# Kernel optimization log

Measured on AMD Instinct MI355X. Metric: run time of the kernel, lower is better.

The kernel has to match this reference:

```python
import jax, jax.numpy as jnp
import numpy as np

K = 4          # deform conv kernel size
STRIDE = 4     # deform conv stride (no padding)
EPS = 1e-5     # BatchNorm eps
SLOPE = 0.01   # LeakyReLU default negative slope


def conv2d(x, w, b, stride):
    out = jax.lax.conv_general_dilated(
        x, w, (stride, stride), 'VALID',
        dimension_numbers=('NCHW', 'OIHW', 'NCHW'))
    return out + b[None, :, None, None]


def batchnorm(x, g, b, m, v):
    inv = g / jnp.sqrt(v + EPS)
    return x * inv[None, :, None, None] + (b - m * inv)[None, :, None, None]


def leaky_relu(x):
    return jnp.where(x >= 0, x, SLOPE * x)


def deform_conv(x, offset, w, b):
    # x: [B,C,H,W], offset: [B,2*K*K,Ho,Wo] with (dy,dx) interleaved per kernel tap
    B, C, H, W = x.shape
    Ho, Wo = offset.shape[2], offset.shape[3]
    KK = K * K
    off = offset.reshape(B, KK, 2, Ho, Wo)
    kh = jnp.repeat(jnp.arange(K), K).astype(x.dtype)   # [KK] kernel row
    kw = jnp.tile(jnp.arange(K), K).astype(x.dtype)     # [KK] kernel col
    base_y = (jnp.arange(Ho) * STRIDE).astype(x.dtype)
    base_x = (jnp.arange(Wo) * STRIDE).astype(x.dtype)
    # sampling coordinates [B,KK,Ho,Wo]
    py = base_y[None, None, :, None] + kh[None, :, None, None] + off[:, :, 0]
    px = base_x[None, None, None, :] + kw[None, :, None, None] + off[:, :, 1]
    y0 = jnp.floor(py)
    x0 = jnp.floor(px)
    wy = py - y0
    wx = px - x0

    def corner(yc, xc):
        yi = yc.astype(jnp.int32)
        xi = xc.astype(jnp.int32)
        valid = (yi >= 0) & (yi < H) & (xi >= 0) & (xi < W)
        yi = jnp.clip(yi, 0, H - 1)
        xi = jnp.clip(xi, 0, W - 1)
        # per-batch gather: [B,C,KK,Ho,Wo]
        v = jax.vmap(lambda img, a, c: img[:, a, c])(x, yi, xi)
        return v * valid[:, None].astype(x.dtype)

    v00 = corner(y0, x0)
    v01 = corner(y0, x0 + 1)
    v10 = corner(y0 + 1, x0)
    v11 = corner(y0 + 1, x0 + 1)
    wy_ = wy[:, None]
    wx_ = wx[:, None]
    sampled = (v00 * (1 - wy_) * (1 - wx_) + v01 * (1 - wy_) * wx_
               + v10 * wy_ * (1 - wx_) + v11 * wy_ * wx_)  # [B,C,KK,Ho,Wo]
    out = jnp.einsum('bckhw,ock->bohw', sampled, w.reshape(w.shape[0], C, KK))
    return out + b[None, :, None, None]


def setup_inputs() -> dict:
    key = jax.random.key(0)
    ks = jax.random.split(key, 16)
    f32 = jnp.float32
    inp = {
        'x': jax.random.normal(ks[0], (64, 3, 224, 224), f32),
        'stem_w': jax.random.normal(ks[1], (96, 3, 4, 4), f32) * 0.1,
        'stem_b': jax.random.normal(ks[2], (96,), f32) * 0.05,
        'bn1_g': jax.random.uniform(ks[3], (96,), f32, 0.5, 1.5),
        'bn1_b': jax.random.normal(ks[4], (96,), f32) * 0.05,
        'bn1_m': jax.random.normal(ks[5], (96,), f32) * 0.05,
        'bn1_v': jax.random.uniform(ks[6], (96,), f32, 0.5, 1.5),
        'off_w': jax.random.normal(ks[7], (32, 96, 4, 4), f32) * 0.02,
        'off_b': jax.random.normal(ks[8], (32,), f32) * 0.02,
        'dcn_w': jax.random.normal(ks[9], (768, 96, 4, 4), f32) * 0.05,
        'dcn_b': jax.random.normal(ks[10], (768,), f32) * 0.05,
        'bn2_g': jax.random.uniform(ks[11], (768,), f32, 0.5, 1.5),
        'bn2_b': jax.random.normal(ks[12], (768,), f32) * 0.05,
        'bn2_m': jax.random.normal(ks[13], (768,), f32) * 0.05,
        'bn2_v': jax.random.uniform(ks[14], (768,), f32, 0.5, 1.5),
    }
    return inp


def reference(x, stem_w, stem_b, bn1_g, bn1_b, bn1_m, bn1_v,
              off_w, off_b, dcn_w, dcn_b, bn2_g, bn2_b, bn2_m, bn2_v):
    h = conv2d(x, stem_w, stem_b, 4)                      # [B,96,56,56]
    h = leaky_relu(batchnorm(h, bn1_g, bn1_b, bn1_m, bn1_v))
    offset = conv2d(h, off_w, off_b, 4)                   # [B,32,14,14]
    h = deform_conv(h, offset, dcn_w, dcn_b)              # [B,768,14,14]
    h = leaky_relu(batchnorm(h, bn2_g, bn2_b, bn2_m, bn2_v))
    B, C, Ho, Wo = h.shape
    return h.reshape(B, C, Ho * Wo).transpose(0, 2, 1)    # [B,196,768]
```

## Files before the change

### kernel.cpp

```cpp
#include <hip/hip_runtime.h>

#define EPS   1e-5f
#define SLOPE 0.01f

#define WS_H1B  0L
#define WS_OFF  9633792L
#define WS_S1   10035200L
#define WS_T1   10035296L
#define WS_T2   10035392L
#define WS_SB   10036160L
#define WS_WTB  19669952L
#define WS_WOB  20259776L
#define WS_W1B  20284352L

__device__ __forceinline__ unsigned short f2bf(float f) {
    unsigned int u = __builtin_bit_cast(unsigned int, f);
    u += 0x7fffu + ((u >> 16) & 1u);
    return (unsigned short)(u >> 16);
}
__device__ __forceinline__ float bf2f(unsigned short u) {
    unsigned int t = ((unsigned int)u) << 16;
    return __builtin_bit_cast(float, t);
}

typedef __attribute__((ext_vector_type(4))) unsigned short ushort4v;
typedef __attribute__((ext_vector_type(8))) unsigned short ushort8v;
typedef __attribute__((ext_vector_type(8))) short bf16x8;
typedef __attribute__((ext_vector_type(4))) float floatx4;

__global__ __launch_bounds__(256) void k0_prep(
    const float* __restrict__ stem_w, const float* __restrict__ stem_b,
    const float* __restrict__ bn1_g,  const float* __restrict__ bn1_b,
    const float* __restrict__ bn1_m,  const float* __restrict__ bn1_v,
    const float* __restrict__ off_w,  const float* __restrict__ dcn_w,
    const float* __restrict__ dcn_b,  const float* __restrict__ bn2_g,
    const float* __restrict__ bn2_b,  const float* __restrict__ bn2_m,
    const float* __restrict__ bn2_v,  float* __restrict__ ws)
{
    long i = (long)blockIdx.x * 256 + threadIdx.x;
    unsigned short* Wtb = (unsigned short*)(ws + WS_WTB);
    unsigned short* Wob = (unsigned short*)(ws + WS_WOB);
    unsigned short* W1b = (unsigned short*)(ws + WS_W1B);
    if (i < 1179648L) {
        int oc = (int)(i / 1536), k = (int)(i % 1536);
        int kk = k / 96, c = k % 96;
        float inv2 = bn2_g[oc] * rsqrtf(bn2_v[oc] + EPS);
        Wtb[i] = f2bf(dcn_w[oc * 1536 + c * 16 + kk] * inv2);
    } else if (i < 1228800L) {
        int i2 = (int)(i - 1179648L);
        int oc = i2 / 1536, k = i2 % 1536;
        int khw = k / 96, c = k % 96;
        Wob[i2] = f2bf(off_w[oc * 1536 + c * 16 + khw]);
    } else if (i < 1234944L) {
        int i3 = (int)(i - 1228800L);
        int ks = i3 / 3072, rr = i3 % 3072;
        int oc = rr >> 5, kl = rr & 31;
        int k  = ks * 32 + kl;
        W1b[i3] = f2bf(k < 48 ? stem_w[oc * 48 + k] : 0.f);
    } else if (i < 1235040L) {
        int c = (int)(i - 1234944L);
        ws[WS_S1 + c] = bn1_g[c] * rsqrtf(bn1_v[c] + EPS);
    } else if (i < 1235136L) {
        int c = (int)(i - 1235040L);
        float s = bn1_g[c] * rsqrtf(bn1_v[c] + EPS);
        ws[WS_T1 + c] = stem_b[c] * s + bn1_b[c] - bn1_m[c] * s;
    } else if (i < 1235904L) {
        int oc = (int)(i - 1235136L);
        float inv2 = bn2_g[oc] * rsqrtf(bn2_v[oc] + EPS);
        ws[WS_T2 + oc] = dcn_b[oc] * inv2 + bn2_b[oc] - bn2_m[oc] * inv2;
    }
}

__global__ __launch_bounds__(256) void k1_stem_mfma(
    const float* __restrict__ x, const unsigned short* __restrict__ W1b,
    const float* __restrict__ s1, const float* __restrict__ t1,
    unsigned short* __restrict__ h1)
{
    const int tid  = threadIdx.x;
    const int wave = tid >> 6, lane = tid & 63;
    const int m = lane & 15, quad = lane >> 4;
    const int p0 = blockIdx.x * 128;

    __shared__ unsigned short sA[2][128][32];
    __shared__ unsigned short sB[2][96][32];

    {
        unsigned short* sBf = &sB[0][0][0];
#pragma unroll
        for (int i = 0; i < 3; i++) {
            int inst = wave * 3 + i;
            const unsigned short* g = W1b + inst * 512 + lane * 8;
            __builtin_amdgcn_global_load_lds(
                (const __attribute__((address_space(1))) void*)g,
                (__attribute__((address_space(3))) void*)(sBf + inst * 512),
                16, 0, 0);
        }
    }

    {
        int r = tid >> 1, off = 16 + (tid & 1) * 8;
        *(ushort8v*)&sA[1][r][off] = (ushort8v)0;
    }

#pragma unroll
    for (int i = 0; i < 6; i++) {
        int cid = tid + 256 * i;
        int r = cid / 12, s = cid % 12;
        int ci = s >> 2, kh = s & 3;
        int p = p0 + r;
        int b  = p / 3136, rem = p % 3136;
        int oy = rem / 56, ox = rem % 56;
        float4 v = *(const float4*)&x[((long)((b * 3 + ci) * 224 + oy * 4 + kh)) * 224 + ox * 4];
        ushort4v hv;
        hv.x = f2bf(v.x); hv.y = f2bf(v.y); hv.z = f2bf(v.z); hv.w = f2bf(v.w);
        int k0i = ci * 16 + kh * 4;
        *(ushort4v*)&sA[k0i >> 5][r][k0i & 31] = hv;
    }
    __syncthreads();

    bf16x8 bfv[6][2], af[2][2];
#pragma unroll
    for (int j = 0; j < 6; j++)
#pragma unroll
        for (int ks = 0; ks < 2; ks++)
            bfv[j][ks] = *(const bf16x8*)&sB[ks][j * 16 + m][quad * 8];
#pragma unroll
    for (int rt = 0; rt < 2; rt++)
#pragma unroll
        for (int ks = 0; ks < 2; ks++)
            af[rt][ks] = *(const bf16x8*)&sA[ks][wave * 32 + rt * 16 + m][quad * 8];

    floatx4 acc[2][6];
#pragma unroll
    for (int rt = 0; rt < 2; rt++)
#pragma unroll
        for (int j = 0; j < 6; j++) {
            floatx4 a = (floatx4)0.f;
            a = __builtin_amdgcn_mfma_f32_16x16x32_bf16(af[rt][0], bfv[j][0], a, 0, 0, 0);
            a = __builtin_amdgcn_mfma_f32_16x16x32_bf16(af[rt][1], bfv[j][1], a, 0, 0, 0);
            acc[rt][j] = a;
        }

#pragma unroll
    for (int j = 0; j < 6; j++) {
        int c = j * 16 + m;
        float sc = s1[c], bi = t1[c];
#pragma unroll
        for (int rt = 0; rt < 2; rt++)
#pragma unroll
            for (int r = 0; r < 4; r++) {
                long p = p0 + wave * 32 + rt * 16 + quad * 4 + r;
                float v = acc[rt][j][r] * sc + bi;
                v = v >= 0.f ? v : SLOPE * v;
                h1[p * 96 + c] = f2bf(v);
            }
    }
}

__global__ __launch_bounds__(256) void k2_mfma(
    const unsigned short* __restrict__ h1,
    const unsigned short* __restrict__ Wob,
    const float* __restrict__ off_b, float* __restrict__ off)
{
    const int tid  = threadIdx.x;
    const int wave = tid >> 6;
    const int lane = tid & 63;
    const int n0   = blockIdx.x * 128;
    const int m    = lane & 15;
    const int quad = lane >> 4;

    __shared__ unsigned short sA[128 * 32];
    __shared__ unsigned short sB[32 * 32];

    const int skoff = (lane & 3) * 8;
    int n_a = n0 + wave * 32 + (lane >> 2);
    int n_b = n_a + 16;
    int ba = n_a / 196, pa = n_a % 196;
    int bb = n_b / 196, pb = n_b % 196;
    long pixa = ((long)(ba * 56 + (pa / 14) * 4) * 56 + (pa % 14) * 4);
    long pixb = ((long)(bb * 56 + (pb / 14) * 4) * 56 + (pb % 14) * 4);

    const unsigned short* gB = Wob + (long)((wave & 1) * 16 + (lane >> 2)) * 1536 + skoff;
    unsigned short* lA0 = &sA[(wave * 32 +  0) * 32];
    unsigned short* lA1 = &sA[(wave * 32 + 16) * 32];
    unsigned short* lB  = &sB[((wave & 1) * 16) * 32];

    floatx4 acc[2][2];
#pragma unroll
    for (int i = 0; i < 2; i++)
#pragma unroll
        for (int j = 0; j < 2; j++) acc[i][j] = (floatx4)0.f;

    for (int kt = 0; kt < 48; ++kt) {
        int khw = kt / 3;
        int c0  = (kt - khw * 3) * 32;
        int kh  = khw >> 2, kw = khw & 3;
        long eoff = (long)(kh * 56 + kw) * 96 + c0 + skoff;
        const unsigned short* gA0 = h1 + pixa * 96 + eoff;
        const unsigned short* gA1 = h1 + pixb * 96 + eoff;

        __syncthreads();
        __builtin_amdgcn_global_load_lds(
            (const __attribute__((address_space(1))) void*)gA0,
            (__attribute__((address_space(3))) void*)lA0, 16, 0, 0);
        __builtin_amdgcn_global_load_lds(
            (const __attribute__((address_space(1))) void*)gA1,
            (__attribute__((address_space(3))) void*)lA1, 16, 0, 0);
        if (wave < 2)
            __builtin_amdgcn_global_load_lds(
                (const __attribute__((address_space(1))) void*)gB,
                (__attribute__((address_space(3))) void*)lB, 16, 0, 0);
        gB += 32;
        __syncthreads();

        bf16x8 af[2], bfr[2];
#pragma unroll
        for (int i = 0; i < 2; i++)
            af[i] = *(const bf16x8*)&sA[(wave * 32 + i * 16 + m) * 32 + quad * 8];
#pragma unroll
        for (int j = 0; j < 2; j++)
            bfr[j] = *(const bf16x8*)&sB[(j * 16 + m) * 32 + quad * 8];
#pragma unroll
        for (int i = 0; i < 2; i++)
#pragma unroll
            for (int j = 0; j < 2; j++)
                acc[i][j] = __builtin_amdgcn_mfma_f32_16x16x32_bf16(
                    af[i], bfr[j], acc[i][j], 0, 0, 0);
    }

    float tb[2];
#pragma unroll
    for (int j = 0; j < 2; j++) tb[j] = off_b[j * 16 + m];
#pragma unroll
    for (int i = 0; i < 2; i++)
#pragma unroll
        for (int r = 0; r < 4; r++) {
            long n = n0 + wave * 32 + i * 16 + quad * 4 + r;
#pragma unroll
            for (int j = 0; j < 2; j++)
                off[n * 32 + j * 16 + m] = acc[i][j][r] + tb[j];
        }
}

__global__ __launch_bounds__(384) void k3_sample(
    const unsigned short* __restrict__ h1, const float* __restrict__ off,
    unsigned short* __restrict__ S)
{
    const int p = blockIdx.x;
    const int b = blockIdx.y;
    const int y = p / 14, xo = p % 14;
    const int tid = threadIdx.x;
    const int c4 = tid % 24, kk = tid / 24;
    const int kh = kk >> 2, kw = kk & 3;

    const float* ob = off + ((long)(b * 196 + p)) * 32;
    float dy = ob[kk * 2];
    float dx = ob[kk * 2 + 1];

    float py = (float)(y * 4 + kh) + dy;
    float px = (float)(xo * 4 + kw) + dx;
    float y0f = floorf(py), x0f = floorf(px);
    float wy = py - y0f, wx = px - x0f;
    int y0 = (int)y0f, x0 = (int)x0f;
    int y1 = y0 + 1,  x1 = x0 + 1;

    float my0 = (y0 >= 0 && y0 < 56) ? 1.f : 0.f;
    float my1 = (y1 >= 0 && y1 < 56) ? 1.f : 0.f;
    float mx0 = (x0 >= 0 && x0 < 56) ? 1.f : 0.f;
    float mx1 = (x1 >= 0 && x1 < 56) ? 1.f : 0.f;
    int y0c = min(max(y0, 0), 55), y1c = min(max(y1, 0), 55);
    int x0c = min(max(x0, 0), 55), x1c = min(max(x1, 0), 55);

    const unsigned short* hb = h1 + (long)b * 56 * 56 * 96 + c4 * 4;
    ushort4v v00 = *(const ushort4v*)&hb[(y0c * 56 + x0c) * 96];
    ushort4v v01 = *(const ushort4v*)&hb[(y0c * 56 + x1c) * 96];
    ushort4v v10 = *(const ushort4v*)&hb[(y1c * 56 + x0c) * 96];
    ushort4v v11 = *(const ushort4v*)&hb[(y1c * 56 + x1c) * 96];

    float w00 = my0 * mx0 * (1.f - wy) * (1.f - wx);
    float w01 = my0 * mx1 * (1.f - wy) * wx;
    float w10 = my1 * mx0 * wy * (1.f - wx);
    float w11 = my1 * mx1 * wy * wx;

    ushort4v rr;
#pragma unroll
    for (int c = 0; c < 4; c++) {
        float v = bf2f(((unsigned short*)&v00)[c]) * w00
                + bf2f(((unsigned short*)&v01)[c]) * w01
                + bf2f(((unsigned short*)&v10)[c]) * w10
                + bf2f(((unsigned short*)&v11)[c]) * w11;
        ((unsigned short*)&rr)[c] = f2bf(v);
    }

    long n = (long)b * 196 + p;
    *(ushort4v*)&S[n * 1536 + kk * 96 + c4 * 4] = rr;
}

__global__ __launch_bounds__(256) void k4_gemm_mfma(
    const unsigned short* __restrict__ S,
    const unsigned short* __restrict__ Wtb,
    const float* __restrict__ t2, float* __restrict__ out)
{
    const int tid  = threadIdx.x;
    const int wave = tid >> 6;
    const int lane = tid & 63;
    const int oc0 = blockIdx.x * 128;
    const int n0  = blockIdx.y * 128;
    const int wr  = wave >> 1, wc = wave & 1;
    const int m    = lane & 15;
    const int quad = lane >> 4;

    __shared__ unsigned short sA[128 * 32];
    __shared__ unsigned short sB[128 * 32];

    const int srow  = wave * 32 + (lane >> 2);
    const int skoff = (lane & 3) * 8;
    const unsigned short* gA0 = S   + (long)(n0  + srow) * 1536 + skoff;
    const unsigned short* gA1 = gA0 + 16L * 1536;
    const unsigned short* gB0 = Wtb + (long)(oc0 + srow) * 1536 + skoff;
    const unsigned short* gB1 = gB0 + 16L * 1536;
    unsigned short* lA0 = &sA[(wave * 32 +  0) * 32];
    unsigned short* lA1 = &sA[(wave * 32 + 16) * 32];
    unsigned short* lB0 = &sB[(wave * 32 +  0) * 32];
    unsigned short* lB1 = &sB[(wave * 32 + 16) * 32];

    floatx4 acc[4][4];
#pragma unroll
    for (int i = 0; i < 4; i++)
#pragma unroll
        for (int j = 0; j < 4; j++) acc[i][j] = (floatx4)0.f;

    for (int kt = 0; kt < 48; ++kt) {
        __syncthreads();
        __builtin_amdgcn_global_load_lds(
            (const __attribute__((address_space(1))) void*)gA0,
            (__attribute__((address_space(3))) void*)lA0, 16, 0, 0);
        __builtin_amdgcn_global_load_lds(
            (const __attribute__((address_space(1))) void*)gA1,
            (__attribute__((address_space(3))) void*)lA1, 16, 0, 0);
        __builtin_amdgcn_global_load_lds(
            (const __attribute__((address_space(1))) void*)gB0,
            (__attribute__((address_space(3))) void*)lB0, 16, 0, 0);
        __builtin_amdgcn_global_load_lds(
            (const __attribute__((address_space(1))) void*)gB1,
            (__attribute__((address_space(3))) void*)lB1, 16, 0, 0);
        gA0 += 32; gA1 += 32; gB0 += 32; gB1 += 32;
        __syncthreads();

        bf16x8 af[4], bf[4];
#pragma unroll
        for (int i = 0; i < 4; i++)
            af[i] = *(const bf16x8*)&sA[(wr * 64 + i * 16 + m) * 32 + quad * 8];
#pragma unroll
        for (int j = 0; j < 4; j++)
            bf[j] = *(const bf16x8*)&sB[(wc * 64 + j * 16 + m) * 32 + quad * 8];
#pragma unroll
        for (int i = 0; i < 4; i++)
#pragma unroll
            for (int j = 0; j < 4; j++)
                acc[i][j] = __builtin_amdgcn_mfma_f32_16x16x32_bf16(
                    af[i], bf[j], acc[i][j], 0, 0, 0);
    }

    float tb[4];
#pragma unroll
    for (int j = 0; j < 4; j++) tb[j] = t2[oc0 + wc * 64 + j * 16 + m];
#pragma unroll
    for (int i = 0; i < 4; i++) {
#pragma unroll
        for (int r = 0; r < 4; r++) {
            long n = n0 + wr * 64 + i * 16 + quad * 4 + r;
            float* orow = out + n * 768 + oc0 + wc * 64 + m;
#pragma unroll
            for (int j = 0; j < 4; j++) {
                float v = acc[i][j][r] + tb[j];
                orow[j * 16] = v >= 0.f ? v : SLOPE * v;
            }
        }
    }
}

extern "C" void kernel_launch(void* const* d_in, const int* in_sizes, int n_in,
                              void* d_out, int out_size, void* d_ws, size_t ws_size,
                              hipStream_t stream)
{
    const float* x      = (const float*)d_in[0];
    const float* stem_w = (const float*)d_in[1];
    const float* stem_b = (const float*)d_in[2];
    const float* bn1_g  = (const float*)d_in[3];
    const float* bn1_b  = (const float*)d_in[4];
    const float* bn1_m  = (const float*)d_in[5];
    const float* bn1_v  = (const float*)d_in[6];
    const float* off_w  = (const float*)d_in[7];
    const float* off_b  = (const float*)d_in[8];
    const float* dcn_w  = (const float*)d_in[9];
    const float* dcn_b  = (const float*)d_in[10];
    const float* bn2_g  = (const float*)d_in[11];
    const float* bn2_b  = (const float*)d_in[12];
    const float* bn2_m  = (const float*)d_in[13];
    const float* bn2_v  = (const float*)d_in[14];

    float* ws  = (float*)d_ws;
    float* out = (float*)d_out;

    unsigned short* h1  = (unsigned short*)(ws + WS_H1B);
    float* off = ws + WS_OFF;
    float* s1  = ws + WS_S1;
    float* t1  = ws + WS_T1;
    float* t2  = ws + WS_T2;
    unsigned short* Sb  = (unsigned short*)(ws + WS_SB);
    unsigned short* Wtb = (unsigned short*)(ws + WS_WTB);
    unsigned short* Wob = (unsigned short*)(ws + WS_WOB);
    unsigned short* W1b = (unsigned short*)(ws + WS_W1B);

    k0_prep<<<4828, 256, 0, stream>>>(stem_w, stem_b, bn1_g, bn1_b, bn1_m, bn1_v,
                                      off_w, dcn_w, dcn_b, bn2_g, bn2_b, bn2_m,
                                      bn2_v, ws);
    k1_stem_mfma<<<1568, 256, 0, stream>>>(x, W1b, s1, t1, h1);
    k2_mfma<<<98, 256, 0, stream>>>(h1, Wob, off_b, off);
    k3_sample<<<dim3(196, 64), 384, 0, stream>>>(h1, off, Sb);
    k4_gemm_mfma<<<dim3(6, 98), 256, 0, stream>>>(Sb, Wtb, t2, out);
}
```

Before: 223.3 us.

## Coalesce weight prep, stage stem output in LDS, remap and double-buffer GEMM

The prep kernel now gives each block one output-channel row: it loads the row into shared memory and writes bf16 weights with vector stores, replacing scattered per-element gathers. The stem kernel writes its bf16 tile through LDS and stores it to global memory in coalesced 16-byte chunks. Its x-load indexing is also reordered. The final GEMM remaps block IDs to keep neighbouring tiles on the same XCD, and loads two K-slices per barrier pair, halving the number of synchronizations. The costs are extra LDS use and added barriers in the stem kernel.

```diff
diff --git a/kernel.cpp b/kernel.cpp
--- a/kernel.cpp
+++ b/kernel.cpp
@@ -37,37 +37,50 @@
     const float* __restrict__ bn2_b,  const float* __restrict__ bn2_m,
     const float* __restrict__ bn2_v,  float* __restrict__ ws)
 {
-    long i = (long)blockIdx.x * 256 + threadIdx.x;
+    const int tid = threadIdx.x;
+    const int blk = blockIdx.x;
     unsigned short* Wtb = (unsigned short*)(ws + WS_WTB);
     unsigned short* Wob = (unsigned short*)(ws + WS_WOB);
     unsigned short* W1b = (unsigned short*)(ws + WS_W1B);
-    if (i < 1179648L) {
-        int oc = (int)(i / 1536), k = (int)(i % 1536);
-        int kk = k / 96, c = k % 96;
-        float inv2 = bn2_g[oc] * rsqrtf(bn2_v[oc] + EPS);
-        Wtb[i] = f2bf(dcn_w[oc * 1536 + c * 16 + kk] * inv2);
-    } else if (i < 1228800L) {
-        int i2 = (int)(i - 1179648L);
-        int oc = i2 / 1536, k = i2 % 1536;
-        int khw = k / 96, c = k % 96;
-        Wob[i2] = f2bf(off_w[oc * 1536 + c * 16 + khw]);
-    } else if (i < 1234944L) {
-        int i3 = (int)(i - 1228800L);
-        int ks = i3 / 3072, rr = i3 % 3072;
-        int oc = rr >> 5, kl = rr & 31;
-        int k  = ks * 32 + kl;
-        W1b[i3] = f2bf(k < 48 ? stem_w[oc * 48 + k] : 0.f);
-    } else if (i < 1235040L) {
-        int c = (int)(i - 1234944L);
-        ws[WS_S1 + c] = bn1_g[c] * rsqrtf(bn1_v[c] + EPS);
-    } else if (i < 1235136L) {
-        int c = (int)(i - 1235040L);
-        float s = bn1_g[c] * rsqrtf(bn1_v[c] + EPS);
-        ws[WS_T1 + c] = stem_b[c] * s + bn1_b[c] - bn1_m[c] * s;
-    } else if (i < 1235904L) {
-        int oc = (int)(i - 1235136L);
-        float inv2 = bn2_g[oc] * rsqrtf(bn2_v[oc] + EPS);
-        ws[WS_T2 + oc] = dcn_b[oc] * inv2 + bn2_b[oc] - bn2_m[oc] * inv2;
+
+    if (blk < 800) {
+        __shared__ float row[1536];
+        const int oc = (blk < 768) ? blk : blk - 768;
+        const float* src = (blk < 768) ? (dcn_w + (long)oc * 1536)
+                                       : (off_w + (long)oc * 1536);
+        for (int i = tid; i < 1536; i += 256) row[i] = src[i];
+        float sc = 1.f;
+        if (blk < 768) sc = bn2_g[oc] * rsqrtf(bn2_v[oc] + EPS);
+        __syncthreads();
+        if (tid < 192) {
+            int k0 = tid * 8;
+            ushort8v o;
+#pragma unroll
+            for (int t = 0; t < 8; t++) {
+                int k = k0 + t;
+                int kk = k / 96, c = k % 96;
+                ((unsigned short*)&o)[t] = f2bf(row[c * 16 + kk] * sc);
+            }
+            unsigned short* dst = (blk < 768) ? (Wtb + (long)oc * 1536 + k0)
+                                              : (Wob + (long)oc * 1536 + k0);
+            *(ushort8v*)dst = o;
+        }
+    } else {
+        for (int i = tid; i < 6144; i += 256) {
+            int ks = i / 3072, rr = i % 3072;
+            int oc = rr >> 5, kl = rr & 31;
+            int k = ks * 32 + kl;
+            W1b[i] = f2bf(k < 48 ? stem_w[oc * 48 + k] : 0.f);
+        }
+        if (tid < 96) {
+            float s = bn1_g[tid] * rsqrtf(bn1_v[tid] + EPS);
+            ws[WS_S1 + tid] = s;
+            ws[WS_T1 + tid] = stem_b[tid] * s + bn1_b[tid] - bn1_m[tid] * s;
+        }
+        for (int i = tid; i < 768; i += 256) {
+            float inv2 = bn2_g[i] * rsqrtf(bn2_v[i] + EPS);
+            ws[WS_T2 + i] = dcn_b[i] * inv2 + bn2_b[i] - bn2_m[i] * inv2;
+        }
     }
 }
 
@@ -81,40 +94,37 @@
     const int m = lane & 15, quad = lane >> 4;
     const int p0 = blockIdx.x * 128;
 
-    __shared__ unsigned short sA[2][128][32];
-    __shared__ unsigned short sB[2][96][32];
-
-    {
-        unsigned short* sBf = &sB[0][0][0];
-#pragma unroll
-        for (int i = 0; i < 3; i++) {
-            int inst = wave * 3 + i;
-            const unsigned short* g = W1b + inst * 512 + lane * 8;
-            __builtin_amdgcn_global_load_lds(
-                (const __attribute__((address_space(1))) void*)g,
-                (__attribute__((address_space(3))) void*)(sBf + inst * 512),
-                16, 0, 0);
-        }
+    __shared__ unsigned short sm[14336];
+    unsigned short* sA = sm;
+    unsigned short* sB = sm + 8192;
+
+#pragma unroll
+    for (int i = 0; i < 3; i++) {
+        int inst = wave * 3 + i;
+        const unsigned short* g = W1b + inst * 512 + lane * 8;
+        __builtin_amdgcn_global_load_lds(
+            (const __attribute__((address_space(1))) void*)g,
+            (__attribute__((address_space(3))) void*)(sB + inst * 512), 16, 0, 0);
     }
 
     {
         int r = tid >> 1, off = 16 + (tid & 1) * 8;
-        *(ushort8v*)&sA[1][r][off] = (ushort8v)0;
+        *(ushort8v*)&sA[4096 + r * 32 + off] = (ushort8v)0;
     }
 
 #pragma unroll
     for (int i = 0; i < 6; i++) {
-        int cid = tid + 256 * i;
-        int r = cid / 12, s = cid % 12;
+        int unit = i * 256 + tid;
+        int r = unit & 127, s = unit >> 7;
         int ci = s >> 2, kh = s & 3;
         int p = p0 + r;
-        int b  = p / 3136, rem = p % 3136;
+        int b = p / 3136, rem = p % 3136;
         int oy = rem / 56, ox = rem % 56;
         float4 v = *(const float4*)&x[((long)((b * 3 + ci) * 224 + oy * 4 + kh)) * 224 + ox * 4];
         ushort4v hv;
         hv.x = f2bf(v.x); hv.y = f2bf(v.y); hv.z = f2bf(v.z); hv.w = f2bf(v.w);
         int k0i = ci * 16 + kh * 4;
-        *(ushort4v*)&sA[k0i >> 5][r][k0i & 31] = hv;
+        *(ushort4v*)&sA[(k0i >> 5) * 4096 + r * 32 + (k0i & 31)] = hv;
     }
     __syncthreads();
 
@@ -123,12 +133,12 @@
     for (int j = 0; j < 6; j++)
 #pragma unroll
         for (int ks = 0; ks < 2; ks++)
-            bfv[j][ks] = *(const bf16x8*)&sB[ks][j * 16 + m][quad * 8];
+            bfv[j][ks] = *(const bf16x8*)&sB[ks * 3072 + (j * 16 + m) * 32 + quad * 8];
 #pragma unroll
     for (int rt = 0; rt < 2; rt++)
 #pragma unroll
         for (int ks = 0; ks < 2; ks++)
-            af[rt][ks] = *(const bf16x8*)&sA[ks][wave * 32 + rt * 16 + m][quad * 8];
+            af[rt][ks] = *(const bf16x8*)&sA[ks * 4096 + (wave * 32 + rt * 16 + m) * 32 + quad * 8];
 
     floatx4 acc[2][6];
 #pragma unroll
@@ -141,6 +151,7 @@
             acc[rt][j] = a;
         }
 
+    __syncthreads();
 #pragma unroll
     for (int j = 0; j < 6; j++) {
         int c = j * 16 + m;
@@ -149,11 +160,17 @@
         for (int rt = 0; rt < 2; rt++)
 #pragma unroll
             for (int r = 0; r < 4; r++) {
-                long p = p0 + wave * 32 + rt * 16 + quad * 4 + r;
+                int row = wave * 32 + rt * 16 + quad * 4 + r;
                 float v = acc[rt][j][r] * sc + bi;
                 v = v >= 0.f ? v : SLOPE * v;
-                h1[p * 96 + c] = f2bf(v);
+                sm[row * 96 + c] = f2bf(v);
             }
+    }
+    __syncthreads();
+#pragma unroll
+    for (int i = 0; i < 6; i++) {
+        int idx = (i * 256 + tid) * 8;
+        *(ushort8v*)&h1[(long)p0 * 96 + idx] = *(const ushort8v*)&sm[idx];
     }
 }
 
@@ -304,14 +321,19 @@
     const int tid  = threadIdx.x;
     const int wave = tid >> 6;
     const int lane = tid & 63;
-    const int oc0 = blockIdx.x * 128;
-    const int n0  = blockIdx.y * 128;
+
+    int lid = blockIdx.x + blockIdx.y * 6;
+    int xcd = lid & 7, s = lid >> 3;
+    int work = (xcd < 4) ? (xcd * 74 + s) : (296 + (xcd - 4) * 73 + s);
+    const int oc0 = (work % 6) * 128;
+    const int n0  = (work / 6) * 128;
+
     const int wr  = wave >> 1, wc = wave & 1;
     const int m    = lane & 15;
     const int quad = lane >> 4;
 
-    __shared__ unsigned short sA[128 * 32];
-    __shared__ unsigned short sB[128 * 32];
+    __shared__ unsigned short sA[2][128 * 32];
+    __shared__ unsigned short sB[2][128 * 32];
 
     const int srow  = wave * 32 + (lane >> 2);
     const int skoff = (lane & 3) * 8;
@@ -319,10 +341,11 @@
     const unsigned short* gA1 = gA0 + 16L * 1536;
     const unsigned short* gB0 = Wtb + (long)(oc0 + srow) * 1536 + skoff;
     const unsigned short* gB1 = gB0 + 16L * 1536;
-    unsigned short* lA0 = &sA[(wave * 32 +  0) * 32];
-    unsigned short* lA1 = &sA[(wave * 32 + 16) * 32];
-    unsigned short* lB0 = &sB[(wave * 32 +  0) * 32];
-    unsigned short* lB1 = &sB[(wave * 32 + 16) * 32];
+    unsigned short* lA0 = &sA[0][(wave * 32 +  0) * 32];
+    unsigned short* lA1 = &sA[0][(wave * 32 + 16) * 32];
+    unsigned short* lB0 = &sB[0][(wave * 32 +  0) * 32];
+    unsigned short* lB1 = &sB[0][(wave * 32 + 16) * 32];
+    const int bufstride = 128 * 32;
 
     floatx4 acc[4][4];
 #pragma unroll
@@ -330,7 +353,7 @@
 #pragma unroll
         for (int j = 0; j < 4; j++) acc[i][j] = (floatx4)0.f;
 
-    for (int kt = 0; kt < 48; ++kt) {
+    for (int kt = 0; kt < 24; ++kt) {
         __syncthreads();
         __builtin_amdgcn_global_load_lds(
             (const __attribute__((address_space(1))) void*)gA0,
@@ -344,22 +367,37 @@
         __builtin_amdgcn_global_load_lds(
             (const __attribute__((address_space(1))) void*)gB1,
             (__attribute__((address_space(3))) void*)lB1, 16, 0, 0);
-        gA0 += 32; gA1 += 32; gB0 += 32; gB1 += 32;
+        __builtin_amdgcn_global_load_lds(
+            (const __attribute__((address_space(1))) void*)(gA0 + 32),
+            (__attribute__((address_space(3))) void*)(lA0 + bufstride), 16, 0, 0);
+        __builtin_amdgcn_global_load_lds(
+            (const __attribute__((address_space(1))) void*)(gA1 + 32),
+            (__attribute__((address_space(3))) void*)(lA1 + bufstride), 16, 0, 0);
+        __builtin_amdgcn_global_load_lds(
+            (const __attribute__((address_space(1))) void*)(gB0 + 32),
+            (__attribute__((address_space(3))) void*)(lB0 + bufstride), 16, 0, 0);
+        __builtin_amdgcn_global_load_lds(
+            (const __attribute__((address_space(1))) void*)(gB1 + 32),
+            (__attribute__((address_space(3))) void*)(lB1 + bufstride), 16, 0, 0);
+        gA0 += 64; gA1 += 64; gB0 += 64; gB1 += 64;
         __syncthreads();
 
-        bf16x8 af[4], bf[4];
-#pragma unroll
-        for (int i = 0; i < 4; i++)
-            af[i] = *(const bf16x8*)&sA[(wr * 64 + i * 16 + m) * 32 + quad * 8];
-#pragma unroll
-        for (int j = 0; j < 4; j++)
-            bf[j] = *(const bf16x8*)&sB[(wc * 64 + j * 16 + m) * 32 + quad * 8];
-#pragma unroll
-        for (int i = 0; i < 4; i++)
+#pragma unroll
+        for (int h = 0; h < 2; h++) {
+            bf16x8 af[4], bf[4];
+#pragma unroll
+            for (int i = 0; i < 4; i++)
+                af[i] = *(const bf16x8*)&sA[h][(wr * 64 + i * 16 + m) * 32 + quad * 8];
 #pragma unroll
             for (int j = 0; j < 4; j++)
-                acc[i][j] = __builtin_amdgcn_mfma_f32_16x16x32_bf16(
-                    af[i], bf[j], acc[i][j], 0, 0, 0);
+                bf[j] = *(const bf16x8*)&sB[h][(wc * 64 + j * 16 + m) * 32 + quad * 8];
+#pragma unroll
+            for (int i = 0; i < 4; i++)
+#pragma unroll
+                for (int j = 0; j < 4; j++)
+                    acc[i][j] = __builtin_amdgcn_mfma_f32_16x16x32_bf16(
+                        af[i], bf[j], acc[i][j], 0, 0, 0);
+        }
     }
 
     float tb[4];
@@ -413,9 +451,9 @@
     unsigned short* Wob = (unsigned short*)(ws + WS_WOB);
     unsigned short* W1b = (unsigned short*)(ws + WS_W1B);
 
-    k0_prep<<<4828, 256, 0, stream>>>(stem_w, stem_b, bn1_g, bn1_b, bn1_m, bn1_v,
-                                      off_w, dcn_w, dcn_b, bn2_g, bn2_b, bn2_m,
-                                      bn2_v, ws);
+    k0_prep<<<801, 256, 0, stream>>>(stem_w, stem_b, bn1_g, bn1_b, bn1_m, bn1_v,
+                                     off_w, dcn_w, dcn_b, bn2_g, bn2_b, bn2_m,
+                                     bn2_v, ws);
     k1_stem_mfma<<<1568, 256, 0, stream>>>(x, W1b, s1, t1, h1);
     k2_mfma<<<98, 256, 0, stream>>>(h1, Wob, off_b, off);
     k3_sample<<<dim3(196, 64), 384, 0, stream>>>(h1, off, Sb);
```

After: 224.2 us. About the same (+0.4%).
